# Performance work log

Hardware: AMD Instinct MI355X
Metric: run time of the kernel (lower is better)

## Reference

```python
import jax, jax.numpy as jnp
import numpy as np

STRIDE = 4
EPS = 1e-6  # torch.pairwise_distance default eps


def setup_inputs() -> dict:
    key = jax.random.key(0)
    k1, k2 = jax.random.split(key)
    a = jax.random.normal(k1, (4, 256, 256, 256), dtype=jnp.float32)
    b = jax.random.normal(k2, (4, 256, 256, 256), dtype=jnp.float32)
    return {"a": a, "b": b}


def _patches(x, stride):
    # nn.Unfold(1, stride): sample every stride-th pixel -> [B, N, C]
    B, C, H, W = x.shape
    xp = x[:, :, ::stride, ::stride]            # [B, C, h, w]
    h, w = xp.shape[2], xp.shape[3]
    return xp.reshape(B, C, h * w).transpose(0, 2, 1), h, w


def reference(a, b):
    B, C, H, W = a.shape
    av, h, w = _patches(a, STRIDE)              # [B, N, C]
    bv, _, _ = _patches(b, STRIDE)              # [B, M, C]
    a2 = jnp.sum(av * av, axis=-1)              # [B, N]
    b2 = jnp.sum(bv * bv, axis=-1)              # [B, M]
    ab = jnp.einsum('bnc,bmc->bnm', av, bv)     # [B, N, M]
    sa = jnp.sum(av, axis=-1)
    sb = jnp.sum(bv, axis=-1)
    d2 = (a2[:, :, None] + b2[:, None, :] - 2.0 * ab
          + 2.0 * EPS * (sa[:, :, None] - sb[:, None, :]) + C * EPS * EPS)
    d2min = jnp.min(d2, axis=-1)                # sqrt is monotone -> min of d2 first
    l2 = jnp.sqrt(jnp.maximum(d2min, 0.0))      # [B, N]
    scores = 2.0 * jax.nn.sigmoid(-l2)
    sm = scores.reshape(B, h, w)
    # F.interpolate(..., mode='nearest') with integer scale == pixel repeat
    out = jnp.repeat(jnp.repeat(sm, STRIDE, axis=1), STRIDE, axis=2)
    return out[:, None, :, :]                   # [B, 1, H, W]
```

## Files before the change

kernel.cpp:

```cpp
#include <hip/hip_runtime.h>
#include <math.h>


#define BATCH 4
#define CH    256
#define HH    256
#define WW    256
#define NPTS  4096
#define EPSV  1e-6f

typedef _Float16 half8  __attribute__((ext_vector_type(8)));
typedef float    f32x4  __attribute__((ext_vector_type(4)));

typedef __attribute__((address_space(1))) const void global_cvoid;
typedef __attribute__((address_space(3))) void lds_void;

#define AC_OFF   0u
#define BC_OFF   (8u << 20)
#define A2_OFF   (16u << 20)
#define B2_OFF   ((16u << 20) + (64u << 10))
#define DP_OFF   ((16u << 20) + (128u << 10))
#define WS_TOTAL ((16u << 20) + (384u << 10))

__global__ __launch_bounds__(256) void gm_gather(
    const float* __restrict__ srcA, const float* __restrict__ srcB,
    unsigned char* __restrict__ ws)
{
  const int t  = threadIdx.x;
  const int h  = blockIdx.x;
  const int b  = blockIdx.y;
  const int z  = blockIdx.z;
  const int w  = t & 63;
  const int wv = t >> 6;

  const float* src = z ? srcB : srcA;
  unsigned char* dst = ws + (z ? BC_OFF : AC_OFF);
  float* norms = (float*)(ws + (z ? B2_OFF : A2_OFF));
  const float epsSign = z ? -2.0f * EPSV : 2.0f * EPSV;
  const float addC    = z ? (float)CH * EPSV * EPSV : 0.0f;

  const float* rowbase = src + ((size_t)b * CH) * (HH * WW)
                             + (size_t)(h * 4) * WW + (size_t)(w * 4);
  float ssum = 0.0f, ssq = 0.0f;
  #pragma unroll
  for (int i = 0; i < 8; ++i) {
    const int kc = wv * 8 + i;
    half8 hv;
    #pragma unroll
    for (int j = 0; j < 8; ++j) {
      const int c = kc * 8 + j;
      float v = rowbase[(size_t)c * (HH * WW)];
      ssum += v;
      ssq  = fmaf(v, v, ssq);
      hv[j] = (_Float16)v;
    }
    *reinterpret_cast<half8*>(dst + ((size_t)((b * 32 + kc) * NPTS + h * 64 + w)) * 16) = hv;
  }

  __shared__ float red[2][4][64];
  red[0][wv][w] = ssum;
  red[1][wv][w] = ssq;
  __syncthreads();
  if (t < 64) {
    float sm = red[0][0][t] + red[0][1][t] + red[0][2][t] + red[0][3][t];
    float sq = red[1][0][t] + red[1][1][t] + red[1][2][t] + red[1][3][t];
    norms[b * NPTS + h * 64 + t] = fmaf(epsSign, sm, sq) + addC;
  }
}

__device__ __forceinline__ void stage_b_tile(const unsigned char* __restrict__ Bc,
                                             int b, int mbase,
                                             unsigned char* dst, int t) {
  const int wv = t >> 6;
  #pragma unroll
  for (int r = 0; r < 4; ++r) {
    unsigned x  = (unsigned)(r * 512 + t) * 16;
    unsigned lb = x ^ (((x >> 9) & 7) << 4);
    unsigned m_l = lb >> 9;
    unsigned kcb = (lb & 511) >> 4;
    const unsigned char* srcp =
        Bc + ((size_t)((b * 32 + kcb) * NPTS + mbase + m_l)) * 16;
    __builtin_amdgcn_global_load_lds((global_cvoid*)srcp,
                                     (lds_void*)(dst + (r * 8192 + wv * 1024)),
                                     16, 0, 0);
  }
}

__global__ __launch_bounds__(512, 2) void gm_gemm_min(
    const unsigned char* __restrict__ Ac, const unsigned char* __restrict__ Bc,
    const float* __restrict__ a2p, const float* __restrict__ b2pc,
    float* __restrict__ d2part)
{
  __shared__ __align__(16) unsigned char smem[131072];
  __shared__ float sB2[1024];

  const int t  = threadIdx.x;
  const int l  = t & 63;
  const int wv = t >> 6;
  const int q  = (l >> 4) & 3;

  const int orig    = blockIdx.x;
  const int logical = (orig & 7) * 32 + (orig >> 3);
  const int ns = logical & 15;
  const int mq = (logical >> 4) & 3;
  const int b  = logical >> 6;
  const int nbase  = ns * 256;
  const int mstart = mq * 1024;

  #pragma unroll
  for (int r = 0; r < 16; ++r) {
    unsigned x  = (unsigned)(r * 512 + t) * 16;
    unsigned lb = x ^ (((x >> 9) & 7) << 4);
    unsigned n_l = lb >> 9;
    unsigned kcb = (lb & 511) >> 4;
    const unsigned char* srcp =
        Ac + ((size_t)((b * 32 + kcb) * NPTS + nbase + n_l)) * 16;
    __builtin_amdgcn_global_load_lds((global_cvoid*)srcp,
                                     (lds_void*)(smem + (r * 8192 + wv * 1024)),
                                     16, 0, 0);
  }
  sB2[t]       = b2pc[b * NPTS + mstart + t];
  sB2[t + 512] = b2pc[b * NPTS + mstart + t + 512];

  asm volatile("s_waitcnt vmcnt(0) lgkmcnt(0)" ::: "memory");
  __builtin_amdgcn_s_barrier();

  half8 af[2][8];
  #pragma unroll
  for (int nf = 0; nf < 2; ++nf) {
    const unsigned rr = wv * 32 + nf * 16 + (l & 15);
    const unsigned sw = (rr & 7) << 4;
    #pragma unroll
    for (int kk = 0; kk < 8; ++kk)
      af[nf][kk] = *reinterpret_cast<const half8*>(
          smem + ((rr * 512 + q * 16 + kk * 64) ^ sw));
  }
  asm volatile("s_waitcnt lgkmcnt(0)" ::: "memory");
  __builtin_amdgcn_s_barrier();

  float rmin[2][4];
  #pragma unroll
  for (int nf = 0; nf < 2; ++nf)
    #pragma unroll
    for (int r = 0; r < 4; ++r) rmin[nf][r] = 3.0e38f;

  stage_b_tile(Bc, b, mstart +   0, smem,          t);
  stage_b_tile(Bc, b, mstart +  64, smem + 32768,  t);
  stage_b_tile(Bc, b, mstart + 128, smem + 65536,  t);

  for (int mt = 0; mt < 16; ++mt) {
    if (mt <= 13)      asm volatile("s_waitcnt vmcnt(8)" ::: "memory");
    else if (mt == 14) asm volatile("s_waitcnt vmcnt(4)" ::: "memory");
    else               asm volatile("s_waitcnt vmcnt(0)" ::: "memory");
    __builtin_amdgcn_s_barrier();

    if (mt <= 12)
      stage_b_tile(Bc, b, mstart + (mt + 3) * 64,
                   smem + (unsigned)((mt + 3) & 3) * 32768, t);

    const unsigned char* cb = smem + (unsigned)(mt & 3) * 32768;

    f32x4 acc[2][4];
    #pragma unroll
    for (int nf = 0; nf < 2; ++nf)
      #pragma unroll
      for (int ms = 0; ms < 4; ++ms) acc[nf][ms] = (f32x4){0.f, 0.f, 0.f, 0.f};

    __builtin_amdgcn_s_setprio(1);
    #pragma unroll
    for (int kk = 0; kk < 8; ++kk) {
      half8 bf[4];
      #pragma unroll
      for (int ms = 0; ms < 4; ++ms) {
        const unsigned rrB = ms * 16 + (l & 15);
        bf[ms] = *reinterpret_cast<const half8*>(
            cb + ((rrB * 512 + q * 16 + kk * 64) ^ ((rrB & 7) << 4)));
      }
      #pragma unroll
      for (int ms = 0; ms < 4; ++ms) {
        acc[0][ms] = __builtin_amdgcn_mfma_f32_16x16x32_f16(af[0][kk], bf[ms], acc[0][ms], 0, 0, 0);
        acc[1][ms] = __builtin_amdgcn_mfma_f32_16x16x32_f16(af[1][kk], bf[ms], acc[1][ms], 0, 0, 0);
      }
    }
    __builtin_amdgcn_s_setprio(0);

    #pragma unroll
    for (int ms = 0; ms < 4; ++ms) {
      const float bp = sB2[mt * 64 + ms * 16 + (l & 15)];
      #pragma unroll
      for (int r = 0; r < 4; ++r) {
        rmin[0][r] = fminf(rmin[0][r], fmaf(-2.0f, acc[0][ms][r], bp));
        rmin[1][r] = fminf(rmin[1][r], fmaf(-2.0f, acc[1][ms][r], bp));
      }
    }
  }

  #pragma unroll
  for (int nf = 0; nf < 2; ++nf)
    #pragma unroll
    for (int r = 0; r < 4; ++r) {
      float v = rmin[nf][r];
      v = fminf(v, __shfl_xor(v, 1, 64));
      v = fminf(v, __shfl_xor(v, 2, 64));
      v = fminf(v, __shfl_xor(v, 4, 64));
      v = fminf(v, __shfl_xor(v, 8, 64));
      if ((l & 15) == 0) {
        const int n = nbase + wv * 32 + nf * 16 + q * 4 + r;
        d2part[(size_t)(b * NPTS + n) * 4 + mq] = v + a2p[b * NPTS + n];
      }
    }
}

__global__ __launch_bounds__(256) void gm_finalize(
    const float* __restrict__ d2part, float* __restrict__ out)
{
  const int id = blockIdx.x * 256 + threadIdx.x;
  const f32x4 u = *reinterpret_cast<const f32x4*>(d2part + (size_t)id * 4);
  const float d2 = fminf(fminf(u[0], u[1]), fminf(u[2], u[3]));
  const float l2 = sqrtf(fmaxf(d2, 0.0f));
  const float s  = 2.0f / (1.0f + expf(l2));
  const int b = id >> 12;
  const int n = id & 4095;
  const int h = n >> 6, w = n & 63;
  float4 v = make_float4(s, s, s, s);
  float* obase = out + ((size_t)(b * 256 + h * 4)) * 256 + w * 4;
  #pragma unroll
  for (int i = 0; i < 4; ++i)
    *reinterpret_cast<float4*>(obase + (size_t)i * 256) = v;
}

__global__ void gm_sentinel(float* out) { out[0] = 1.0e6f; }

extern "C" void kernel_launch(void* const* d_in, const int* in_sizes, int n_in,
                              void* d_out, int out_size, void* d_ws, size_t ws_size,
                              hipStream_t stream) {
  const float* a = (const float*)d_in[0];
  const float* b = (const float*)d_in[1];
  float* out = (float*)d_out;
  unsigned char* ws = (unsigned char*)d_ws;

  if (ws_size < (size_t)WS_TOTAL) {
    gm_sentinel<<<1, 1, 0, stream>>>(out);
    return;
  }

  gm_gather<<<dim3(64, 4, 2), 256, 0, stream>>>(a, b, ws);
  gm_gemm_min<<<256, 512, 0, stream>>>(
      ws + AC_OFF, ws + BC_OFF,
      (const float*)(ws + A2_OFF), (const float*)(ws + B2_OFF),
      (float*)(ws + DP_OFF));
  gm_finalize<<<64, 256, 0, stream>>>((const float*)(ws + DP_OFF), out);
}
```

Before: 72.71 us.

## Re-tile GEMM-min warps to 64x32 sub-tiles with B fragment prefetch

Each block's eight waves now form a 4x2 grid, each owning 64 A rows by 32 B columns per tile, instead of 32 rows by all 64 columns. This cuts per-wave LDS reads of B fragments, which are now prefetched one k-step ahead. The cost is twice as many resident A fragments (more VGPRs), so the 2-blocks-per-CU launch bound is dropped. The partial-min buffer grows to 8 entries per point and the finalize kernel reduces over 8 values.

```diff
diff --git a/kernel.cpp b/kernel.cpp
--- a/kernel.cpp
+++ b/kernel.cpp
@@ -20,7 +20,7 @@
 #define A2_OFF   (16u << 20)
 #define B2_OFF   ((16u << 20) + (64u << 10))
 #define DP_OFF   ((16u << 20) + (128u << 10))
-#define WS_TOTAL ((16u << 20) + (384u << 10))
+#define WS_TOTAL ((16u << 20) + (640u << 10))
 
 __global__ __launch_bounds__(256) void gm_gather(
     const float* __restrict__ srcA, const float* __restrict__ srcB,
@@ -86,7 +86,7 @@
   }
 }
 
-__global__ __launch_bounds__(512, 2) void gm_gemm_min(
+__global__ __launch_bounds__(512) void gm_gemm_min(
     const unsigned char* __restrict__ Ac, const unsigned char* __restrict__ Bc,
     const float* __restrict__ a2p, const float* __restrict__ b2pc,
     float* __restrict__ d2part)
@@ -97,6 +97,8 @@
   const int t  = threadIdx.x;
   const int l  = t & 63;
   const int wv = t >> 6;
+  const int wn = wv & 3;
+  const int wm = wv >> 2;
   const int q  = (l >> 4) & 3;
 
   const int orig    = blockIdx.x;
@@ -125,10 +127,10 @@
   asm volatile("s_waitcnt vmcnt(0) lgkmcnt(0)" ::: "memory");
   __builtin_amdgcn_s_barrier();
 
-  half8 af[2][8];
-  #pragma unroll
-  for (int nf = 0; nf < 2; ++nf) {
-    const unsigned rr = wv * 32 + nf * 16 + (l & 15);
+  half8 af[4][8];
+  #pragma unroll
+  for (int nf = 0; nf < 4; ++nf) {
+    const unsigned rr = wn * 64 + nf * 16 + (l & 15);
     const unsigned sw = (rr & 7) << 4;
     #pragma unroll
     for (int kk = 0; kk < 8; ++kk)
@@ -138,11 +140,16 @@
   asm volatile("s_waitcnt lgkmcnt(0)" ::: "memory");
   __builtin_amdgcn_s_barrier();
 
-  float rmin[2][4];
-  #pragma unroll
-  for (int nf = 0; nf < 2; ++nf)
+  float rmin[4][4];
+  #pragma unroll
+  for (int nf = 0; nf < 4; ++nf)
     #pragma unroll
     for (int r = 0; r < 4; ++r) rmin[nf][r] = 3.0e38f;
+
+  const unsigned rrB0 = wm * 32 + (l & 15);
+  const unsigned rrB1 = rrB0 + 16;
+  const unsigned swB0 = (rrB0 & 7) << 4;
+  const unsigned swB1 = (rrB1 & 7) << 4;
 
   stage_b_tile(Bc, b, mstart +   0, smem,          t);
   stage_b_tile(Bc, b, mstart +  64, smem + 32768,  t);
@@ -160,43 +167,49 @@
 
     const unsigned char* cb = smem + (unsigned)(mt & 3) * 32768;
 
-    f32x4 acc[2][4];
-    #pragma unroll
-    for (int nf = 0; nf < 2; ++nf)
-      #pragma unroll
-      for (int ms = 0; ms < 4; ++ms) acc[nf][ms] = (f32x4){0.f, 0.f, 0.f, 0.f};
+    f32x4 acc[4][2];
+    #pragma unroll
+    for (int nf = 0; nf < 4; ++nf) {
+      acc[nf][0] = (f32x4){0.f, 0.f, 0.f, 0.f};
+      acc[nf][1] = (f32x4){0.f, 0.f, 0.f, 0.f};
+    }
+
+    half8 b0 = *reinterpret_cast<const half8*>(cb + ((rrB0 * 512 + q * 16) ^ swB0));
+    half8 b1 = *reinterpret_cast<const half8*>(cb + ((rrB1 * 512 + q * 16) ^ swB1));
 
     __builtin_amdgcn_s_setprio(1);
     #pragma unroll
     for (int kk = 0; kk < 8; ++kk) {
-      half8 bf[4];
-      #pragma unroll
-      for (int ms = 0; ms < 4; ++ms) {
-        const unsigned rrB = ms * 16 + (l & 15);
-        bf[ms] = *reinterpret_cast<const half8*>(
-            cb + ((rrB * 512 + q * 16 + kk * 64) ^ ((rrB & 7) << 4)));
+      half8 n0, n1;
+      if (kk < 7) {
+        n0 = *reinterpret_cast<const half8*>(
+            cb + ((rrB0 * 512 + q * 16 + (kk + 1) * 64) ^ swB0));
+        n1 = *reinterpret_cast<const half8*>(
+            cb + ((rrB1 * 512 + q * 16 + (kk + 1) * 64) ^ swB1));
       }
       #pragma unroll
-      for (int ms = 0; ms < 4; ++ms) {
-        acc[0][ms] = __builtin_amdgcn_mfma_f32_16x16x32_f16(af[0][kk], bf[ms], acc[0][ms], 0, 0, 0);
-        acc[1][ms] = __builtin_amdgcn_mfma_f32_16x16x32_f16(af[1][kk], bf[ms], acc[1][ms], 0, 0, 0);
-      }
+      for (int nf = 0; nf < 4; ++nf)
+        acc[nf][0] = __builtin_amdgcn_mfma_f32_16x16x32_f16(af[nf][kk], b0, acc[nf][0], 0, 0, 0);
+      #pragma unroll
+      for (int nf = 0; nf < 4; ++nf)
+        acc[nf][1] = __builtin_amdgcn_mfma_f32_16x16x32_f16(af[nf][kk], b1, acc[nf][1], 0, 0, 0);
+      if (kk < 7) { b0 = n0; b1 = n1; }
     }
     __builtin_amdgcn_s_setprio(0);
 
-    #pragma unroll
-    for (int ms = 0; ms < 4; ++ms) {
-      const float bp = sB2[mt * 64 + ms * 16 + (l & 15)];
+    const float bp0 = sB2[mt * 64 + wm * 32 + (l & 15)];
+    const float bp1 = sB2[mt * 64 + wm * 32 + 16 + (l & 15)];
+    #pragma unroll
+    for (int nf = 0; nf < 4; ++nf)
       #pragma unroll
       for (int r = 0; r < 4; ++r) {
-        rmin[0][r] = fminf(rmin[0][r], fmaf(-2.0f, acc[0][ms][r], bp));
-        rmin[1][r] = fminf(rmin[1][r], fmaf(-2.0f, acc[1][ms][r], bp));
+        rmin[nf][r] = fminf(rmin[nf][r], fmaf(-2.0f, acc[nf][0][r], bp0));
+        rmin[nf][r] = fminf(rmin[nf][r], fmaf(-2.0f, acc[nf][1][r], bp1));
       }
-    }
-  }
-
-  #pragma unroll
-  for (int nf = 0; nf < 2; ++nf)
+  }
+
+  #pragma unroll
+  for (int nf = 0; nf < 4; ++nf)
     #pragma unroll
     for (int r = 0; r < 4; ++r) {
       float v = rmin[nf][r];
@@ -205,8 +218,8 @@
       v = fminf(v, __shfl_xor(v, 4, 64));
       v = fminf(v, __shfl_xor(v, 8, 64));
       if ((l & 15) == 0) {
-        const int n = nbase + wv * 32 + nf * 16 + q * 4 + r;
-        d2part[(size_t)(b * NPTS + n) * 4 + mq] = v + a2p[b * NPTS + n];
+        const int n = nbase + wn * 64 + nf * 16 + q * 4 + r;
+        d2part[(size_t)(b * NPTS + n) * 8 + mq * 2 + wm] = v + a2p[b * NPTS + n];
       }
     }
 }
@@ -215,8 +228,10 @@
     const float* __restrict__ d2part, float* __restrict__ out)
 {
   const int id = blockIdx.x * 256 + threadIdx.x;
-  const f32x4 u = *reinterpret_cast<const f32x4*>(d2part + (size_t)id * 4);
-  const float d2 = fminf(fminf(u[0], u[1]), fminf(u[2], u[3]));
+  const f32x4 u  = *reinterpret_cast<const f32x4*>(d2part + (size_t)id * 8);
+  const f32x4 w4 = *reinterpret_cast<const f32x4*>(d2part + (size_t)id * 8 + 4);
+  const float d2 = fminf(fminf(fminf(u[0], u[1]), fminf(u[2], u[3])),
+                         fminf(fminf(w4[0], w4[1]), fminf(w4[2], w4[3])));
   const float l2 = sqrtf(fmaxf(d2, 0.0f));
   const float s  = 2.0f / (1.0f + expf(l2));
   const int b = id >> 12;
```

Result: no change. 74.09 us (+1.9%).
